# Optimization experiments

Measured on AMD Instinct MI355X. Metric: run time of the kernel, lower is better.

## Reference

```python
import jax, jax.numpy as jnp
import numpy as np
from jax.scipy.special import erf

# synthetic covalent radii table (original imports `covalent_radii`, e.g. from ase)
COV_RADII = jnp.asarray(0.3 + 0.02 * np.arange(100), dtype=jnp.float32)

B_MOL = 1024   # molecules per batch
N_ATOM = 128   # atoms per molecule (equal-sized ragged batch, atoms sorted by molecule)
N_ELEM = 10


def setup_inputs() -> dict:
    key = jax.random.key(0)
    ks = jax.random.split(key, 6)
    N = B_MOL * N_ATOM
    return {
        "eneg": jax.random.normal(ks[0], (N, 1), jnp.float32),
        "positions": jax.random.normal(ks[1], (N, 3), jnp.float32) * 3.0,
        "node_attrs": jax.random.uniform(ks[2], (N, N_ELEM), jnp.float32),
        "hardness": jax.random.uniform(ks[3], (N_ELEM,), jnp.float32),
        "total_charge": jax.random.normal(ks[4], (B_MOL,), jnp.float32),
        "batch": jnp.repeat(jnp.arange(B_MOL), N_ATOM),          # sorted molecule ids
        "atomic_numbers": jax.random.randint(ks[5], (N,), 1, 90),
    }


def reference(eneg, positions, node_attrs, hardness, total_charge, batch, atomic_numbers):
    # atoms are sorted by molecule with equal molecule sizes, so the ragged
    # python loop of the original collapses to a batched [B, n, ...] computation.
    B = total_charge.shape[0]
    N = positions.shape[0]
    n = N // B
    sqrt_pi = jnp.sqrt(jnp.asarray(np.pi, jnp.float32))
    sqrt_2 = jnp.sqrt(jnp.asarray(2.0, jnp.float32))

    pos = positions.reshape(B, n, 3)
    Z = atomic_numbers.reshape(B, n)
    atom_idx = jnp.argmax(node_attrs, axis=1).reshape(B, n)

    r = COV_RADII[Z]                                     # [B, n]
    diag_vals = hardness[atom_idx] + 1.0 / (sqrt_pi * r)  # [B, n]
    sigma = jnp.square(r)                                # [B, n]
    gamma = jnp.sqrt(sigma[:, :, None] + sigma[:, None, :])  # [B, n, n]

    diff = pos[:, :, None, :] - pos[:, None, :, :]       # [B, n, n, 3]
    sq = jnp.sum(diff * diff, axis=-1)                   # [B, n, n]
    eye = jnp.eye(n, dtype=bool)
    dist = jnp.sqrt(jnp.where(eye, 1.0, sq))             # safe diag (overwritten below)

    A = erf(dist / (sqrt_2 * gamma)) / dist              # [B, n, n]
    A = jnp.where(eye, diag_vals[:, :, None], A)         # scatter hardness diagonal

    # augment with charge-conservation row/column of ones (corner = 1)
    A = jnp.concatenate([A, jnp.ones((B, n, 1), A.dtype)], axis=2)
    A = jnp.concatenate([A, jnp.ones((B, 1, n + 1), A.dtype)], axis=1)

    b = jnp.concatenate([-eneg.reshape(B, n, 1),
                         total_charge.reshape(B, 1, 1)], axis=1)  # [B, n+1, 1]

    x = jnp.linalg.solve(A, b)                           # batched small solves
    return x[:, :n, 0].reshape(-1)                       # partial charges, [N]
```

## Files before the change

kernel.cpp:

```cpp
#include <hip/hip_runtime.h>
#include <math.h>

#define NMOL  1024
#define N     128
#define NELEM 10
#define BLOCK 256
#define PW    8
#define NPAN  16
#define PSTR  12
#define USTR  132

typedef __attribute__((ext_vector_type(4))) float f4;


__global__ __launch_bounds__(BLOCK, 2) void ceq_solve_kernel(
    const float* __restrict__ eneg,
    const float* __restrict__ positions,
    const float* __restrict__ node_attrs,
    const float* __restrict__ hardness,
    const float* __restrict__ total_charge,
    const int*   __restrict__ atomic_numbers,
    float* __restrict__ out)
{
    __shared__ __align__(16) float P[2][N * PSTR];
    __shared__ __align__(16) float Up[2][PW * USTR];
    __shared__ __align__(16) float Ublk[2][NPAN][PW][PW];
    __shared__ float rhsY[2][N], rhsZ[2][N];
    __shared__ float sxY[2][N], sxZ[2][N];
    __shared__ float px[2][N], py[2][N], pz[2][N], sg[2][N], dgv[2][N];
    __shared__ float lamS[2];

    const int tid  = threadIdx.x;
    const int lane = tid & 63;
    const int wid  = tid >> 6;
    const int g    = tid >> 7;
    const int wv   = wid & 1;
    const int gt   = tid & 127;
    const int r0   = 2 * lane;
    const int r1   = r0 + 1;
    const int col0 = 64 * wv;
    const int mol  = 2 * blockIdx.x + g;
    const int base = mol * N;

    {
        const int i = gt;
        const int Z = atomic_numbers[base + i];
        const float rad = 0.3f + 0.02f * (float)Z;
        sg[g][i] = rad * rad;
        const float* na = node_attrs + (size_t)(base + i) * NELEM;
        float best = na[0]; int bi = 0;
        #pragma unroll
        for (int e = 1; e < NELEM; ++e) {
            float v = na[e];
            if (v > best) { best = v; bi = e; }
        }
        dgv[g][i] = hardness[bi] + 0.5641895835477563f / rad;
        const float* p = positions + (size_t)(base + i) * 3;
        px[g][i] = p[0]; py[g][i] = p[1]; pz[g][i] = p[2];
        rhsY[g][i] = -eneg[base + i];
        rhsZ[g][i] = 1.0f;
    }
    __syncthreads();

    f4 Ar0[16], Ar1[16];
    {
        const float x0 = px[g][r0], y0 = py[g][r0], z0 = pz[g][r0];
        const float s0 = sg[g][r0], d0 = dgv[g][r0];
        #pragma unroll
        for (int c = 0; c < 16; ++c) {
            f4 v0;
            #pragma unroll
            for (int e = 0; e < 4; ++e) {
                const int j = col0 + 4 * c + e;
                float a0;
                if (j == r0) a0 = d0;
                else {
                    const float dx = x0 - px[g][j], dy = y0 - py[g][j], dz = z0 - pz[g][j];
                    const float d = sqrtf(dx * dx + dy * dy + dz * dz);
                    a0 = erff(d / (1.4142135623730951f * sqrtf(s0 + sg[g][j]))) / d;
                }
                ((float*)&v0)[e] = a0;
            }
            Ar0[c] = v0;
        }
        const float x1 = px[g][r1], y1 = py[g][r1], z1 = pz[g][r1];
        const float s1 = sg[g][r1], d1 = dgv[g][r1];
        #pragma unroll
        for (int c = 0; c < 16; ++c) {
            f4 v1;
            #pragma unroll
            for (int e = 0; e < 4; ++e) {
                const int j = col0 + 4 * c + e;
                float a1;
                if (j == r1) a1 = d1;
                else {
                    const float dx = x1 - px[g][j], dy = y1 - py[g][j], dz = z1 - pz[g][j];
                    const float d = sqrtf(dx * dx + dy * dy + dz * dz);
                    a1 = erff(d / (1.4142135623730951f * sqrtf(s1 + sg[g][j]))) / d;
                }
                ((float*)&v1)[e] = a1;
            }
            Ar1[c] = v1;
        }
    }

    for (int p = 0; p < NPAN; ++p) {
        const int k0   = PW * p;
        const int gclo = 2 * p + 2;
        const int q    = p & 7;

        if (wv == (p >> 3) && lane >= 4 * p) {
            f4 a00, a01, a10, a11;
            switch (q) {
                case 0:  a00 = Ar0[0];  a01 = Ar0[1];  a10 = Ar1[0];  a11 = Ar1[1];  break;
                case 1:  a00 = Ar0[2];  a01 = Ar0[3];  a10 = Ar1[2];  a11 = Ar1[3];  break;
                case 2:  a00 = Ar0[4];  a01 = Ar0[5];  a10 = Ar1[4];  a11 = Ar1[5];  break;
                case 3:  a00 = Ar0[6];  a01 = Ar0[7];  a10 = Ar1[6];  a11 = Ar1[7];  break;
                case 4:  a00 = Ar0[8];  a01 = Ar0[9];  a10 = Ar1[8];  a11 = Ar1[9];  break;
                case 5:  a00 = Ar0[10]; a01 = Ar0[11]; a10 = Ar1[10]; a11 = Ar1[11]; break;
                case 6:  a00 = Ar0[12]; a01 = Ar0[13]; a10 = Ar1[12]; a11 = Ar1[13]; break;
                default: a00 = Ar0[14]; a01 = Ar0[15]; a10 = Ar1[14]; a11 = Ar1[15]; break;
            }
            *(f4*)&P[g][r0 * PSTR + 0] = a00; *(f4*)&P[g][r0 * PSTR + 4] = a01;
            *(f4*)&P[g][r1 * PSTR + 0] = a10; *(f4*)&P[g][r1 * PSTR + 4] = a11;
        }
        if (lane >= 4 * p && lane < 4 * p + 4) {
            const int u0 = r0 - k0, u1 = u0 + 1;
            #pragma unroll
            for (int c = 0; c < 16; ++c) {
                const int gc = 16 * wv + c;
                if (gc >= gclo) {
                    *(f4*)&Up[g][u0 * USTR + 4 * gc] = Ar0[c];
                    *(f4*)&Up[g][u1 * USTR + 4 * gc] = Ar1[c];
                }
            }
        }
        if (gt < PW) {
            Up[g][gt * USTR + 128] = rhsY[g][k0 + gt];
            Up[g][gt * USTR + 129] = rhsZ[g][k0 + gt];
        }
        __syncthreads();

        if (wv == 0) {
            const int i0 = k0 + lane, i1 = i0 + 64;
            const bool v0 = i0 < N, v1 = i1 < N;
            float rg0[PW], rg1[PW];
            if (v0) {
                f4 a = *(const f4*)&P[g][i0 * PSTR], b = *(const f4*)&P[g][i0 * PSTR + 4];
                rg0[0]=a.x; rg0[1]=a.y; rg0[2]=a.z; rg0[3]=a.w;
                rg0[4]=b.x; rg0[5]=b.y; rg0[6]=b.z; rg0[7]=b.w;
            } else {
                #pragma unroll
                for (int j = 0; j < PW; ++j) rg0[j] = 0.0f;
            }
            if (v1) {
                f4 a = *(const f4*)&P[g][i1 * PSTR], b = *(const f4*)&P[g][i1 * PSTR + 4];
                rg1[0]=a.x; rg1[1]=a.y; rg1[2]=a.z; rg1[3]=a.w;
                rg1[4]=b.x; rg1[5]=b.y; rg1[6]=b.z; rg1[7]=b.w;
            } else {
                #pragma unroll
                for (int j = 0; j < PW; ++j) rg1[j] = 0.0f;
            }
            #pragma unroll
            for (int kk = 0; kk < PW; ++kk) {
                float pr[PW];
                #pragma unroll
                for (int j = kk; j < PW; ++j) pr[j] = __shfl(rg0[j], kk);
                const float dinv = 1.0f / pr[kk];
                if (v0 && i0 > k0 + kk) {
                    const float mult = rg0[kk] * dinv; rg0[kk] = mult;
                    #pragma unroll
                    for (int j = kk + 1; j < PW; ++j) rg0[j] -= mult * pr[j];
                }
                if (v1) {
                    const float mult = rg1[kk] * dinv; rg1[kk] = mult;
                    #pragma unroll
                    for (int j = kk + 1; j < PW; ++j) rg1[j] -= mult * pr[j];
                }
            }
            if (v0) {
                f4 a = { rg0[0], rg0[1], rg0[2], rg0[3] };
                f4 b = { rg0[4], rg0[5], rg0[6], rg0[7] };
                *(f4*)&P[g][i0 * PSTR] = a; *(f4*)&P[g][i0 * PSTR + 4] = b;
                if (lane < PW) {
                    *(f4*)&Ublk[g][p][lane][0] = a; *(f4*)&Ublk[g][p][lane][4] = b;
                }
            }
            if (v1) {
                f4 a = { rg1[0], rg1[1], rg1[2], rg1[3] };
                f4 b = { rg1[4], rg1[5], rg1[6], rg1[7] };
                *(f4*)&P[g][i1 * PSTR] = a; *(f4*)&P[g][i1 * PSTR + 4] = b;
            }
        }
        __syncthreads();

        const int ncols = 122 - k0;
        if (gt < ncols) {
            const int j = k0 + PW + gt;
            float u[PW];
            #pragma unroll
            for (int kk = 0; kk < PW; ++kk) u[kk] = Up[g][kk * USTR + j];
            #pragma unroll
            for (int kk = 1; kk < PW; ++kk) {
                float acc = u[kk];
                #pragma unroll
                for (int t = 0; t < kk; ++t) acc -= Ublk[g][p][kk][t] * u[t];
                u[kk] = acc;
            }
            #pragma unroll
            for (int kk = 0; kk < PW; ++kk) Up[g][kk * USTR + j] = u[kk];
        }
        __syncthreads();

        if (lane >= 4 * p && lane < 4 * p + 4) {
            const int u0 = r0 - k0, u1 = u0 + 1;
            #pragma unroll
            for (int c = 0; c < 16; ++c) {
                const int gc = 16 * wv + c;
                if (gc >= gclo) {
                    Ar0[c] = *(const f4*)&Up[g][u0 * USTR + 4 * gc];
                    Ar1[c] = *(const f4*)&Up[g][u1 * USTR + 4 * gc];
                }
            }
        }
        if (gt < PW) {
            rhsY[g][k0 + gt] = Up[g][gt * USTR + 128];
            rhsZ[g][k0 + gt] = Up[g][gt * USTR + 129];
        }
        const bool hasmat = (16 * wv + 15) >= gclo;
        if (lane >= 4 * p + 4) {
            float lA0[PW], lA1[PW];
            if (hasmat || wv == 0) {
                f4 a = *(const f4*)&P[g][r0 * PSTR], b = *(const f4*)&P[g][r0 * PSTR + 4];
                lA0[0]=a.x; lA0[1]=a.y; lA0[2]=a.z; lA0[3]=a.w;
                lA0[4]=b.x; lA0[5]=b.y; lA0[6]=b.z; lA0[7]=b.w;
                f4 c2 = *(const f4*)&P[g][r1 * PSTR], d2 = *(const f4*)&P[g][r1 * PSTR + 4];
                lA1[0]=c2.x; lA1[1]=c2.y; lA1[2]=c2.z; lA1[3]=c2.w;
                lA1[4]=d2.x; lA1[5]=d2.y; lA1[6]=d2.z; lA1[7]=d2.w;
            }
            if (hasmat) {
                #pragma unroll
                for (int c = 0; c < 16; ++c) {
                    const int gc = 16 * wv + c;
                    if (gc >= gclo) {
                        f4 acc0 = Ar0[c], acc1 = Ar1[c];
                        #pragma unroll
                        for (int u = 0; u < PW; ++u) {
                            const f4 uv = *(const f4*)&Up[g][u * USTR + 4 * gc];
                            acc0 -= uv * lA0[u];
                            acc1 -= uv * lA1[u];
                        }
                        Ar0[c] = acc0; Ar1[c] = acc1;
                    }
                }
            }
            if (wv == 0) {
                float yy0 = rhsY[g][r0], yy1 = rhsY[g][r1];
                float zz0 = rhsZ[g][r0], zz1 = rhsZ[g][r1];
                #pragma unroll
                for (int u = 0; u < PW; ++u) {
                    const float uy = Up[g][u * USTR + 128];
                    const float uz = Up[g][u * USTR + 129];
                    yy0 -= lA0[u] * uy; yy1 -= lA1[u] * uy;
                    zz0 -= lA0[u] * uz; zz1 -= lA1[u] * uz;
                }
                rhsY[g][r0] = yy0; rhsY[g][r1] = yy1;
                rhsZ[g][r0] = zz0; rhsZ[g][r1] = zz1;
            }
        }
        __syncthreads();
    }

    for (int pb = NPAN - 1; pb >= 0; --pb) {
        const int k0 = PW * pb;
        if (tid < 4) {
            const int gg = tid >> 1;
            float* rhs = (tid & 1) ? rhsZ[gg] : rhsY[gg];
            float* sx  = (tid & 1) ? sxZ[gg]  : sxY[gg];
            float x[PW];
            #pragma unroll
            for (int kk = PW - 1; kk >= 0; --kk) {
                float acc = rhs[k0 + kk];
                #pragma unroll
                for (int jj = kk + 1; jj < PW; ++jj) acc -= Ublk[gg][pb][kk][jj] * x[jj];
                x[kk] = acc / Ublk[gg][pb][kk][kk];
                sx[k0 + kk] = x[kk];
            }
        }
        __syncthreads();
        if (wv == (pb >> 3) && lane < 4 * pb) {
            f4 a00, a01, a10, a11;
            switch (pb & 7) {
                case 0:  a00 = Ar0[0];  a01 = Ar0[1];  a10 = Ar1[0];  a11 = Ar1[1];  break;
                case 1:  a00 = Ar0[2];  a01 = Ar0[3];  a10 = Ar1[2];  a11 = Ar1[3];  break;
                case 2:  a00 = Ar0[4];  a01 = Ar0[5];  a10 = Ar1[4];  a11 = Ar1[5];  break;
                case 3:  a00 = Ar0[6];  a01 = Ar0[7];  a10 = Ar1[6];  a11 = Ar1[7];  break;
                case 4:  a00 = Ar0[8];  a01 = Ar0[9];  a10 = Ar1[8];  a11 = Ar1[9];  break;
                case 5:  a00 = Ar0[10]; a01 = Ar0[11]; a10 = Ar1[10]; a11 = Ar1[11]; break;
                case 6:  a00 = Ar0[12]; a01 = Ar0[13]; a10 = Ar1[12]; a11 = Ar1[13]; break;
                default: a00 = Ar0[14]; a01 = Ar0[15]; a10 = Ar1[14]; a11 = Ar1[15]; break;
            }
            float yy0 = rhsY[g][r0], yy1 = rhsY[g][r1];
            float zz0 = rhsZ[g][r0], zz1 = rhsZ[g][r1];
            yy0 -= a00.x*sxY[g][k0]   + a00.y*sxY[g][k0+1] + a00.z*sxY[g][k0+2] + a00.w*sxY[g][k0+3]
                 + a01.x*sxY[g][k0+4] + a01.y*sxY[g][k0+5] + a01.z*sxY[g][k0+6] + a01.w*sxY[g][k0+7];
            yy1 -= a10.x*sxY[g][k0]   + a10.y*sxY[g][k0+1] + a10.z*sxY[g][k0+2] + a10.w*sxY[g][k0+3]
                 + a11.x*sxY[g][k0+4] + a11.y*sxY[g][k0+5] + a11.z*sxY[g][k0+6] + a11.w*sxY[g][k0+7];
            zz0 -= a00.x*sxZ[g][k0]   + a00.y*sxZ[g][k0+1] + a00.z*sxZ[g][k0+2] + a00.w*sxZ[g][k0+3]
                 + a01.x*sxZ[g][k0+4] + a01.y*sxZ[g][k0+5] + a01.z*sxZ[g][k0+6] + a01.w*sxZ[g][k0+7];
            zz1 -= a10.x*sxZ[g][k0]   + a10.y*sxZ[g][k0+1] + a10.z*sxZ[g][k0+2] + a10.w*sxZ[g][k0+3]
                 + a11.x*sxZ[g][k0+4] + a11.y*sxZ[g][k0+5] + a11.z*sxZ[g][k0+6] + a11.w*sxZ[g][k0+7];
            rhsY[g][r0] = yy0; rhsY[g][r1] = yy1;
            rhsZ[g][r0] = zz0; rhsZ[g][r1] = zz1;
        }
        __syncthreads();
    }

    if (wv == 0) {
        float vY = sxY[g][lane] + sxY[g][lane + 64];
        float vZ = sxZ[g][lane] + sxZ[g][lane + 64];
        #pragma unroll
        for (int off = 32; off; off >>= 1) {
            vY += __shfl_xor(vY, off);
            vZ += __shfl_xor(vZ, off);
        }
        if (lane == 0) lamS[g] = (vY - total_charge[mol]) / (vZ - 1.0f);
    }
    __syncthreads();
    out[base + gt] = sxY[g][gt] - lamS[g] * sxZ[g][gt];
}

extern "C" void kernel_launch(void* const* d_in, const int* in_sizes, int n_in,
                              void* d_out, int out_size, void* d_ws, size_t ws_size,
                              hipStream_t stream) {
    const float* eneg           = (const float*)d_in[0];
    const float* positions      = (const float*)d_in[1];
    const float* node_attrs     = (const float*)d_in[2];
    const float* hardness       = (const float*)d_in[3];
    const float* total_charge   = (const float*)d_in[4];
    const int*   atomic_numbers = (const int*)d_in[6];
    float* out = (float*)d_out;

    ceq_solve_kernel<<<NMOL / 2, BLOCK, 0, stream>>>(
        eneg, positions, node_attrs, hardness, total_charge, atomic_numbers, out);
}
```

Baseline: 226.3 us.

## Double-buffer panel and U-row staging to drop a barrier per panel step

Panel columns and next U rows are now written into a second shared buffer directly from the trailing update of the previous step. The separate staging phase and its __syncthreads at the top of each panel iteration go away. The right-hand sides are kept in registers instead of shared arrays, and the launch-bounds occupancy hint of 2 is removed. The cost is more shared memory for the doubled P/Up buffers and extra conditional stores inside the update loop.

```diff
diff --git a/kernel.cpp b/kernel.cpp
--- a/kernel.cpp
+++ b/kernel.cpp
@@ -13,7 +13,7 @@
 typedef __attribute__((ext_vector_type(4))) float f4;
 
 
-__global__ __launch_bounds__(BLOCK, 2) void ceq_solve_kernel(
+__global__ __launch_bounds__(BLOCK) void ceq_solve_kernel(
     const float* __restrict__ eneg,
     const float* __restrict__ positions,
     const float* __restrict__ node_attrs,
@@ -22,8 +22,8 @@
     const int*   __restrict__ atomic_numbers,
     float* __restrict__ out)
 {
-    __shared__ __align__(16) float P[2][N * PSTR];
-    __shared__ __align__(16) float Up[2][PW * USTR];
+    __shared__ __align__(16) float P[2][2][N * PSTR];
+    __shared__ __align__(16) float Up[2][2][PW * USTR];
     __shared__ __align__(16) float Ublk[2][NPAN][PW][PW];
     __shared__ float rhsY[2][N], rhsZ[2][N];
     __shared__ float sxY[2][N], sxZ[2][N];
@@ -57,9 +57,9 @@
         dgv[g][i] = hardness[bi] + 0.5641895835477563f / rad;
         const float* p = positions + (size_t)(base + i) * 3;
         px[g][i] = p[0]; py[g][i] = p[1]; pz[g][i] = p[2];
-        rhsY[g][i] = -eneg[base + i];
-        rhsZ[g][i] = 1.0f;
-    }
+    }
+    float rY0 = 0.f, rY1 = 0.f, rZ0 = 1.f, rZ1 = 1.f;
+    if (wv == 0) { rY0 = -eneg[base + r0]; rY1 = -eneg[base + r1]; }
     __syncthreads();
 
     f4 Ar0[16], Ar1[16];
@@ -104,59 +104,50 @@
         }
     }
 
+    if (wv == 0) {
+        *(f4*)&P[g][0][r0 * PSTR + 0] = Ar0[0]; *(f4*)&P[g][0][r0 * PSTR + 4] = Ar0[1];
+        *(f4*)&P[g][0][r1 * PSTR + 0] = Ar1[0]; *(f4*)&P[g][0][r1 * PSTR + 4] = Ar1[1];
+    }
+    if (lane < 4) {
+        #pragma unroll
+        for (int c = 0; c < 16; ++c) {
+            const int gc = 16 * wv + c;
+            if (gc >= 2) {
+                *(f4*)&Up[g][0][r0 * USTR + 4 * gc] = Ar0[c];
+                *(f4*)&Up[g][0][r1 * USTR + 4 * gc] = Ar1[c];
+            }
+        }
+        if (wv == 0) {
+            Up[g][0][r0 * USTR + 128] = rY0; Up[g][0][r1 * USTR + 128] = rY1;
+            Up[g][0][r0 * USTR + 129] = rZ0; Up[g][0][r1 * USTR + 129] = rZ1;
+        }
+    }
+    __syncthreads();
+
     for (int p = 0; p < NPAN; ++p) {
         const int k0   = PW * p;
         const int gclo = 2 * p + 2;
-        const int q    = p & 7;
-
-        if (wv == (p >> 3) && lane >= 4 * p) {
-            f4 a00, a01, a10, a11;
-            switch (q) {
-                case 0:  a00 = Ar0[0];  a01 = Ar0[1];  a10 = Ar1[0];  a11 = Ar1[1];  break;
-                case 1:  a00 = Ar0[2];  a01 = Ar0[3];  a10 = Ar1[2];  a11 = Ar1[3];  break;
-                case 2:  a00 = Ar0[4];  a01 = Ar0[5];  a10 = Ar1[4];  a11 = Ar1[5];  break;
-                case 3:  a00 = Ar0[6];  a01 = Ar0[7];  a10 = Ar1[6];  a11 = Ar1[7];  break;
-                case 4:  a00 = Ar0[8];  a01 = Ar0[9];  a10 = Ar1[8];  a11 = Ar1[9];  break;
-                case 5:  a00 = Ar0[10]; a01 = Ar0[11]; a10 = Ar1[10]; a11 = Ar1[11]; break;
-                case 6:  a00 = Ar0[12]; a01 = Ar0[13]; a10 = Ar1[12]; a11 = Ar1[13]; break;
-                default: a00 = Ar0[14]; a01 = Ar0[15]; a10 = Ar1[14]; a11 = Ar1[15]; break;
-            }
-            *(f4*)&P[g][r0 * PSTR + 0] = a00; *(f4*)&P[g][r0 * PSTR + 4] = a01;
-            *(f4*)&P[g][r1 * PSTR + 0] = a10; *(f4*)&P[g][r1 * PSTR + 4] = a11;
-        }
-        if (lane >= 4 * p && lane < 4 * p + 4) {
-            const int u0 = r0 - k0, u1 = u0 + 1;
-            #pragma unroll
-            for (int c = 0; c < 16; ++c) {
-                const int gc = 16 * wv + c;
-                if (gc >= gclo) {
-                    *(f4*)&Up[g][u0 * USTR + 4 * gc] = Ar0[c];
-                    *(f4*)&Up[g][u1 * USTR + 4 * gc] = Ar1[c];
-                }
-            }
-        }
-        if (gt < PW) {
-            Up[g][gt * USTR + 128] = rhsY[g][k0 + gt];
-            Up[g][gt * USTR + 129] = rhsZ[g][k0 + gt];
-        }
-        __syncthreads();
+        const int b    = p & 1;
+        const int bn   = b ^ 1;
+        const int pn   = p + 1;
+        const int k0n  = PW * pn;
 
         if (wv == 0) {
             const int i0 = k0 + lane, i1 = i0 + 64;
             const bool v0 = i0 < N, v1 = i1 < N;
             float rg0[PW], rg1[PW];
             if (v0) {
-                f4 a = *(const f4*)&P[g][i0 * PSTR], b = *(const f4*)&P[g][i0 * PSTR + 4];
+                f4 a = *(const f4*)&P[g][b][i0 * PSTR], b2 = *(const f4*)&P[g][b][i0 * PSTR + 4];
                 rg0[0]=a.x; rg0[1]=a.y; rg0[2]=a.z; rg0[3]=a.w;
-                rg0[4]=b.x; rg0[5]=b.y; rg0[6]=b.z; rg0[7]=b.w;
+                rg0[4]=b2.x; rg0[5]=b2.y; rg0[6]=b2.z; rg0[7]=b2.w;
             } else {
                 #pragma unroll
                 for (int j = 0; j < PW; ++j) rg0[j] = 0.0f;
             }
             if (v1) {
-                f4 a = *(const f4*)&P[g][i1 * PSTR], b = *(const f4*)&P[g][i1 * PSTR + 4];
+                f4 a = *(const f4*)&P[g][b][i1 * PSTR], b2 = *(const f4*)&P[g][b][i1 * PSTR + 4];
                 rg1[0]=a.x; rg1[1]=a.y; rg1[2]=a.z; rg1[3]=a.w;
-                rg1[4]=b.x; rg1[5]=b.y; rg1[6]=b.z; rg1[7]=b.w;
+                rg1[4]=b2.x; rg1[5]=b2.y; rg1[6]=b2.z; rg1[7]=b2.w;
             } else {
                 #pragma unroll
                 for (int j = 0; j < PW; ++j) rg1[j] = 0.0f;
@@ -180,16 +171,16 @@
             }
             if (v0) {
                 f4 a = { rg0[0], rg0[1], rg0[2], rg0[3] };
-                f4 b = { rg0[4], rg0[5], rg0[6], rg0[7] };
-                *(f4*)&P[g][i0 * PSTR] = a; *(f4*)&P[g][i0 * PSTR + 4] = b;
+                f4 b2 = { rg0[4], rg0[5], rg0[6], rg0[7] };
+                *(f4*)&P[g][b][i0 * PSTR] = a; *(f4*)&P[g][b][i0 * PSTR + 4] = b2;
                 if (lane < PW) {
-                    *(f4*)&Ublk[g][p][lane][0] = a; *(f4*)&Ublk[g][p][lane][4] = b;
+                    *(f4*)&Ublk[g][p][lane][0] = a; *(f4*)&Ublk[g][p][lane][4] = b2;
                 }
             }
             if (v1) {
                 f4 a = { rg1[0], rg1[1], rg1[2], rg1[3] };
-                f4 b = { rg1[4], rg1[5], rg1[6], rg1[7] };
-                *(f4*)&P[g][i1 * PSTR] = a; *(f4*)&P[g][i1 * PSTR + 4] = b;
+                f4 b2 = { rg1[4], rg1[5], rg1[6], rg1[7] };
+                *(f4*)&P[g][b][i1 * PSTR] = a; *(f4*)&P[g][b][i1 * PSTR + 4] = b2;
             }
         }
         __syncthreads();
@@ -199,7 +190,7 @@
             const int j = k0 + PW + gt;
             float u[PW];
             #pragma unroll
-            for (int kk = 0; kk < PW; ++kk) u[kk] = Up[g][kk * USTR + j];
+            for (int kk = 0; kk < PW; ++kk) u[kk] = Up[g][b][kk * USTR + j];
             #pragma unroll
             for (int kk = 1; kk < PW; ++kk) {
                 float acc = u[kk];
@@ -208,7 +199,7 @@
                 u[kk] = acc;
             }
             #pragma unroll
-            for (int kk = 0; kk < PW; ++kk) Up[g][kk * USTR + j] = u[kk];
+            for (int kk = 0; kk < PW; ++kk) Up[g][b][kk * USTR + j] = u[kk];
         }
         __syncthreads();
 
@@ -218,23 +209,24 @@
             for (int c = 0; c < 16; ++c) {
                 const int gc = 16 * wv + c;
                 if (gc >= gclo) {
-                    Ar0[c] = *(const f4*)&Up[g][u0 * USTR + 4 * gc];
-                    Ar1[c] = *(const f4*)&Up[g][u1 * USTR + 4 * gc];
+                    Ar0[c] = *(const f4*)&Up[g][b][u0 * USTR + 4 * gc];
+                    Ar1[c] = *(const f4*)&Up[g][b][u1 * USTR + 4 * gc];
                 }
             }
         }
         if (gt < PW) {
-            rhsY[g][k0 + gt] = Up[g][gt * USTR + 128];
-            rhsZ[g][k0 + gt] = Up[g][gt * USTR + 129];
+            rhsY[g][k0 + gt] = Up[g][b][gt * USTR + 128];
+            rhsZ[g][k0 + gt] = Up[g][b][gt * USTR + 129];
         }
         const bool hasmat = (16 * wv + 15) >= gclo;
+        const bool nown   = (lane >= 4 * pn && lane < 4 * pn + 4);
         if (lane >= 4 * p + 4) {
             float lA0[PW], lA1[PW];
             if (hasmat || wv == 0) {
-                f4 a = *(const f4*)&P[g][r0 * PSTR], b = *(const f4*)&P[g][r0 * PSTR + 4];
+                f4 a = *(const f4*)&P[g][b][r0 * PSTR], b2 = *(const f4*)&P[g][b][r0 * PSTR + 4];
                 lA0[0]=a.x; lA0[1]=a.y; lA0[2]=a.z; lA0[3]=a.w;
-                lA0[4]=b.x; lA0[5]=b.y; lA0[6]=b.z; lA0[7]=b.w;
-                f4 c2 = *(const f4*)&P[g][r1 * PSTR], d2 = *(const f4*)&P[g][r1 * PSTR + 4];
+                lA0[4]=b2.x; lA0[5]=b2.y; lA0[6]=b2.z; lA0[7]=b2.w;
+                f4 c2 = *(const f4*)&P[g][b][r1 * PSTR], d2 = *(const f4*)&P[g][b][r1 * PSTR + 4];
                 lA1[0]=c2.x; lA1[1]=c2.y; lA1[2]=c2.z; lA1[3]=c2.w;
                 lA1[4]=d2.x; lA1[5]=d2.y; lA1[6]=d2.z; lA1[7]=d2.w;
             }
@@ -246,26 +238,40 @@
                         f4 acc0 = Ar0[c], acc1 = Ar1[c];
                         #pragma unroll
                         for (int u = 0; u < PW; ++u) {
-                            const f4 uv = *(const f4*)&Up[g][u * USTR + 4 * gc];
+                            const f4 uv = *(const f4*)&Up[g][b][u * USTR + 4 * gc];
                             acc0 -= uv * lA0[u];
                             acc1 -= uv * lA1[u];
                         }
                         Ar0[c] = acc0; Ar1[c] = acc1;
+                        if (p < NPAN - 1) {
+                            if (gc == 2 * pn) {
+                                *(f4*)&P[g][bn][r0 * PSTR + 0] = acc0;
+                                *(f4*)&P[g][bn][r1 * PSTR + 0] = acc1;
+                            } else if (gc == 2 * pn + 1) {
+                                *(f4*)&P[g][bn][r0 * PSTR + 4] = acc0;
+                                *(f4*)&P[g][bn][r1 * PSTR + 4] = acc1;
+                            } else if (nown) {
+                                *(f4*)&Up[g][bn][(r0 - k0n) * USTR + 4 * gc] = acc0;
+                                *(f4*)&Up[g][bn][(r1 - k0n) * USTR + 4 * gc] = acc1;
+                            }
+                        }
                     }
                 }
             }
             if (wv == 0) {
-                float yy0 = rhsY[g][r0], yy1 = rhsY[g][r1];
-                float zz0 = rhsZ[g][r0], zz1 = rhsZ[g][r1];
                 #pragma unroll
                 for (int u = 0; u < PW; ++u) {
-                    const float uy = Up[g][u * USTR + 128];
-                    const float uz = Up[g][u * USTR + 129];
-                    yy0 -= lA0[u] * uy; yy1 -= lA1[u] * uy;
-                    zz0 -= lA0[u] * uz; zz1 -= lA1[u] * uz;
-                }
-                rhsY[g][r0] = yy0; rhsY[g][r1] = yy1;
-                rhsZ[g][r0] = zz0; rhsZ[g][r1] = zz1;
+                    const float uy = Up[g][b][u * USTR + 128];
+                    const float uz = Up[g][b][u * USTR + 129];
+                    rY0 -= lA0[u] * uy; rY1 -= lA1[u] * uy;
+                    rZ0 -= lA0[u] * uz; rZ1 -= lA1[u] * uz;
+                }
+                if (p < NPAN - 1 && nown) {
+                    Up[g][bn][(r0 - k0n) * USTR + 128] = rY0;
+                    Up[g][bn][(r1 - k0n) * USTR + 128] = rY1;
+                    Up[g][bn][(r0 - k0n) * USTR + 129] = rZ0;
+                    Up[g][bn][(r1 - k0n) * USTR + 129] = rZ1;
+                }
             }
         }
         __syncthreads();
```

Measured after the change: 335.6 us. 48.3% more time.

## Spill first four matrix column-chunks to LDS and factor panel from U-row copy

Applied to the files above, without the earlier changes.

Moves the first 4 of 16 per-thread f4 column chunks of the in-register matrix into shared memory, so fewer registers are held and occupancy or spill behaviour may improve. It also drops the P panel buffer. The 8x8 diagonal block is now factored by 8 lanes reading the already-published U rows, and the L multipliers are rebuilt from the transposed U row times stored reciprocal pivots. The cost is extra LDS traffic for the spilled chunks and per-row multiplier loads, plus a slightly altered elimination structure.

```diff
diff --git a/kernel.cpp b/kernel.cpp
--- a/kernel.cpp
+++ b/kernel.cpp
@@ -7,7 +7,6 @@
 #define BLOCK 256
 #define PW    8
 #define NPAN  16
-#define PSTR  12
 #define USTR  132
 
 typedef __attribute__((ext_vector_type(4))) float f4;
@@ -22,9 +21,11 @@
     const int*   __restrict__ atomic_numbers,
     float* __restrict__ out)
 {
-    __shared__ __align__(16) float P[2][N * PSTR];
+    __shared__ __align__(16) f4    Aex0[4][BLOCK];
+    __shared__ __align__(16) f4    Aex1[4][BLOCK];
     __shared__ __align__(16) float Up[2][PW * USTR];
     __shared__ __align__(16) float Ublk[2][NPAN][PW][PW];
+    __shared__ float dinvS[2][PW];
     __shared__ float rhsY[2][N], rhsZ[2][N];
     __shared__ float sxY[2][N], sxZ[2][N];
     __shared__ float px[2][N], py[2][N], pz[2][N], sg[2][N], dgv[2][N];
@@ -62,7 +63,7 @@
     }
     __syncthreads();
 
-    f4 Ar0[16], Ar1[16];
+    f4 Ar0[12], Ar1[12];
     {
         const float x0 = px[g][r0], y0 = py[g][r0], z0 = pz[g][r0];
         const float s0 = sg[g][r0], d0 = dgv[g][r0];
@@ -81,7 +82,7 @@
                 }
                 ((float*)&v0)[e] = a0;
             }
-            Ar0[c] = v0;
+            if (c < 4) Aex0[c][tid] = v0; else Ar0[c - 4] = v0;
         }
         const float x1 = px[g][r1], y1 = py[g][r1], z1 = pz[g][r1];
         const float s1 = sg[g][r1], d1 = dgv[g][r1];
@@ -100,38 +101,31 @@
                 }
                 ((float*)&v1)[e] = a1;
             }
-            Ar1[c] = v1;
-        }
-    }
+            if (c < 4) Aex1[c][tid] = v1; else Ar1[c - 4] = v1;
+        }
+    }
+    __syncthreads();
 
     for (int p = 0; p < NPAN; ++p) {
         const int k0   = PW * p;
         const int gclo = 2 * p + 2;
-        const int q    = p & 7;
-
-        if (wv == (p >> 3) && lane >= 4 * p) {
-            f4 a00, a01, a10, a11;
-            switch (q) {
-                case 0:  a00 = Ar0[0];  a01 = Ar0[1];  a10 = Ar1[0];  a11 = Ar1[1];  break;
-                case 1:  a00 = Ar0[2];  a01 = Ar0[3];  a10 = Ar1[2];  a11 = Ar1[3];  break;
-                case 2:  a00 = Ar0[4];  a01 = Ar0[5];  a10 = Ar1[4];  a11 = Ar1[5];  break;
-                case 3:  a00 = Ar0[6];  a01 = Ar0[7];  a10 = Ar1[6];  a11 = Ar1[7];  break;
-                case 4:  a00 = Ar0[8];  a01 = Ar0[9];  a10 = Ar1[8];  a11 = Ar1[9];  break;
-                case 5:  a00 = Ar0[10]; a01 = Ar0[11]; a10 = Ar1[10]; a11 = Ar1[11]; break;
-                case 6:  a00 = Ar0[12]; a01 = Ar0[13]; a10 = Ar1[12]; a11 = Ar1[13]; break;
-                default: a00 = Ar0[14]; a01 = Ar0[15]; a10 = Ar1[14]; a11 = Ar1[15]; break;
-            }
-            *(f4*)&P[g][r0 * PSTR + 0] = a00; *(f4*)&P[g][r0 * PSTR + 4] = a01;
-            *(f4*)&P[g][r1 * PSTR + 0] = a10; *(f4*)&P[g][r1 * PSTR + 4] = a11;
-        }
+
         if (lane >= 4 * p && lane < 4 * p + 4) {
             const int u0 = r0 - k0, u1 = u0 + 1;
             #pragma unroll
-            for (int c = 0; c < 16; ++c) {
+            for (int c = 0; c < 4; ++c) {
                 const int gc = 16 * wv + c;
-                if (gc >= gclo) {
-                    *(f4*)&Up[g][u0 * USTR + 4 * gc] = Ar0[c];
-                    *(f4*)&Up[g][u1 * USTR + 4 * gc] = Ar1[c];
+                if (gc >= 2 * p) {
+                    *(f4*)&Up[g][u0 * USTR + 4 * gc] = Aex0[c][tid];
+                    *(f4*)&Up[g][u1 * USTR + 4 * gc] = Aex1[c][tid];
+                }
+            }
+            #pragma unroll
+            for (int c = 4; c < 16; ++c) {
+                const int gc = 16 * wv + c;
+                if (gc >= 2 * p) {
+                    *(f4*)&Up[g][u0 * USTR + 4 * gc] = Ar0[c - 4];
+                    *(f4*)&Up[g][u1 * USTR + 4 * gc] = Ar1[c - 4];
                 }
             }
         }
@@ -141,56 +135,25 @@
         }
         __syncthreads();
 
-        if (wv == 0) {
-            const int i0 = k0 + lane, i1 = i0 + 64;
-            const bool v0 = i0 < N, v1 = i1 < N;
-            float rg0[PW], rg1[PW];
-            if (v0) {
-                f4 a = *(const f4*)&P[g][i0 * PSTR], b = *(const f4*)&P[g][i0 * PSTR + 4];
-                rg0[0]=a.x; rg0[1]=a.y; rg0[2]=a.z; rg0[3]=a.w;
-                rg0[4]=b.x; rg0[5]=b.y; rg0[6]=b.z; rg0[7]=b.w;
-            } else {
-                #pragma unroll
-                for (int j = 0; j < PW; ++j) rg0[j] = 0.0f;
-            }
-            if (v1) {
-                f4 a = *(const f4*)&P[g][i1 * PSTR], b = *(const f4*)&P[g][i1 * PSTR + 4];
-                rg1[0]=a.x; rg1[1]=a.y; rg1[2]=a.z; rg1[3]=a.w;
-                rg1[4]=b.x; rg1[5]=b.y; rg1[6]=b.z; rg1[7]=b.w;
-            } else {
-                #pragma unroll
-                for (int j = 0; j < PW; ++j) rg1[j] = 0.0f;
-            }
+        if (wv == 0 && lane < PW) {
+            float v[PW];
+            #pragma unroll
+            for (int t = 0; t < PW; ++t) v[t] = Up[g][lane * USTR + k0 + t];
             #pragma unroll
             for (int kk = 0; kk < PW; ++kk) {
                 float pr[PW];
                 #pragma unroll
-                for (int j = kk; j < PW; ++j) pr[j] = __shfl(rg0[j], kk);
-                const float dinv = 1.0f / pr[kk];
-                if (v0 && i0 > k0 + kk) {
-                    const float mult = rg0[kk] * dinv; rg0[kk] = mult;
+                for (int j = kk; j < PW; ++j) pr[j] = __shfl(v[j], kk);
+                if (lane > kk) {
+                    const float mult = v[kk] / pr[kk];
+                    v[kk] = mult;
                     #pragma unroll
-                    for (int j = kk + 1; j < PW; ++j) rg0[j] -= mult * pr[j];
-                }
-                if (v1) {
-                    const float mult = rg1[kk] * dinv; rg1[kk] = mult;
-                    #pragma unroll
-                    for (int j = kk + 1; j < PW; ++j) rg1[j] -= mult * pr[j];
-                }
-            }
-            if (v0) {
-                f4 a = { rg0[0], rg0[1], rg0[2], rg0[3] };
-                f4 b = { rg0[4], rg0[5], rg0[6], rg0[7] };
-                *(f4*)&P[g][i0 * PSTR] = a; *(f4*)&P[g][i0 * PSTR + 4] = b;
-                if (lane < PW) {
-                    *(f4*)&Ublk[g][p][lane][0] = a; *(f4*)&Ublk[g][p][lane][4] = b;
-                }
-            }
-            if (v1) {
-                f4 a = { rg1[0], rg1[1], rg1[2], rg1[3] };
-                f4 b = { rg1[4], rg1[5], rg1[6], rg1[7] };
-                *(f4*)&P[g][i1 * PSTR] = a; *(f4*)&P[g][i1 * PSTR + 4] = b;
-            }
+                    for (int j = kk + 1; j < PW; ++j) v[j] -= mult * pr[j];
+                }
+            }
+            #pragma unroll
+            for (int t = 0; t < PW; ++t) Ublk[g][p][lane][t] = v[t];
+            dinvS[g][lane] = 1.0f / v[lane];
         }
         __syncthreads();
 
@@ -215,11 +178,19 @@
         if (lane >= 4 * p && lane < 4 * p + 4) {
             const int u0 = r0 - k0, u1 = u0 + 1;
             #pragma unroll
-            for (int c = 0; c < 16; ++c) {
+            for (int c = 0; c < 4; ++c) {
                 const int gc = 16 * wv + c;
                 if (gc >= gclo) {
-                    Ar0[c] = *(const f4*)&Up[g][u0 * USTR + 4 * gc];
-                    Ar1[c] = *(const f4*)&Up[g][u1 * USTR + 4 * gc];
+                    Aex0[c][tid] = *(const f4*)&Up[g][u0 * USTR + 4 * gc];
+                    Aex1[c][tid] = *(const f4*)&Up[g][u1 * USTR + 4 * gc];
+                }
+            }
+            #pragma unroll
+            for (int c = 4; c < 16; ++c) {
+                const int gc = 16 * wv + c;
+                if (gc >= gclo) {
+                    Ar0[c - 4] = *(const f4*)&Up[g][u0 * USTR + 4 * gc];
+                    Ar1[c - 4] = *(const f4*)&Up[g][u1 * USTR + 4 * gc];
                 }
             }
         }
@@ -231,26 +202,40 @@
         if (lane >= 4 * p + 4) {
             float lA0[PW], lA1[PW];
             if (hasmat || wv == 0) {
-                f4 a = *(const f4*)&P[g][r0 * PSTR], b = *(const f4*)&P[g][r0 * PSTR + 4];
-                lA0[0]=a.x; lA0[1]=a.y; lA0[2]=a.z; lA0[3]=a.w;
-                lA0[4]=b.x; lA0[5]=b.y; lA0[6]=b.z; lA0[7]=b.w;
-                f4 c2 = *(const f4*)&P[g][r1 * PSTR], d2 = *(const f4*)&P[g][r1 * PSTR + 4];
-                lA1[0]=c2.x; lA1[1]=c2.y; lA1[2]=c2.z; lA1[3]=c2.w;
-                lA1[4]=d2.x; lA1[5]=d2.y; lA1[6]=d2.z; lA1[7]=d2.w;
+                #pragma unroll
+                for (int u = 0; u < PW; ++u) {
+                    const float du = dinvS[g][u];
+                    lA0[u] = Up[g][u * USTR + r0] * du;
+                    lA1[u] = Up[g][u * USTR + r1] * du;
+                }
             }
             if (hasmat) {
                 #pragma unroll
-                for (int c = 0; c < 16; ++c) {
+                for (int c = 0; c < 4; ++c) {
                     const int gc = 16 * wv + c;
                     if (gc >= gclo) {
-                        f4 acc0 = Ar0[c], acc1 = Ar1[c];
+                        f4 acc0 = Aex0[c][tid], acc1 = Aex1[c][tid];
                         #pragma unroll
                         for (int u = 0; u < PW; ++u) {
                             const f4 uv = *(const f4*)&Up[g][u * USTR + 4 * gc];
                             acc0 -= uv * lA0[u];
                             acc1 -= uv * lA1[u];
                         }
-                        Ar0[c] = acc0; Ar1[c] = acc1;
+                        Aex0[c][tid] = acc0; Aex1[c][tid] = acc1;
+                    }
+                }
+                #pragma unroll
+                for (int c = 4; c < 16; ++c) {
+                    const int gc = 16 * wv + c;
+                    if (gc >= gclo) {
+                        f4 acc0 = Ar0[c - 4], acc1 = Ar1[c - 4];
+                        #pragma unroll
+                        for (int u = 0; u < PW; ++u) {
+                            const f4 uv = *(const f4*)&Up[g][u * USTR + 4 * gc];
+                            acc0 -= uv * lA0[u];
+                            acc1 -= uv * lA1[u];
+                        }
+                        Ar0[c - 4] = acc0; Ar1[c - 4] = acc1;
                     }
                 }
             }
@@ -291,14 +276,16 @@
         if (wv == (pb >> 3) && lane < 4 * pb) {
             f4 a00, a01, a10, a11;
             switch (pb & 7) {
-                case 0:  a00 = Ar0[0];  a01 = Ar0[1];  a10 = Ar1[0];  a11 = Ar1[1];  break;
-                case 1:  a00 = Ar0[2];  a01 = Ar0[3];  a10 = Ar1[2];  a11 = Ar1[3];  break;
-                case 2:  a00 = Ar0[4];  a01 = Ar0[5];  a10 = Ar1[4];  a11 = Ar1[5];  break;
-                case 3:  a00 = Ar0[6];  a01 = Ar0[7];  a10 = Ar1[6];  a11 = Ar1[7];  break;
-                case 4:  a00 = Ar0[8];  a01 = Ar0[9];  a10 = Ar1[8];  a11 = Ar1[9];  break;
-                case 5:  a00 = Ar0[10]; a01 = Ar0[11]; a10 = Ar1[10]; a11 = Ar1[11]; break;
-                case 6:  a00 = Ar0[12]; a01 = Ar0[13]; a10 = Ar1[12]; a11 = Ar1[13]; break;
-                default: a00 = Ar0[14]; a01 = Ar0[15]; a10 = Ar1[14]; a11 = Ar1[15]; break;
+                case 0:  a00 = Aex0[0][tid]; a01 = Aex0[1][tid];
+                         a10 = Aex1[0][tid]; a11 = Aex1[1][tid]; break;
+                case 1:  a00 = Aex0[2][tid]; a01 = Aex0[3][tid];
+                         a10 = Aex1[2][tid]; a11 = Aex1[3][tid]; break;
+                case 2:  a00 = Ar0[0];  a01 = Ar0[1];  a10 = Ar1[0];  a11 = Ar1[1];  break;
+                case 3:  a00 = Ar0[2];  a01 = Ar0[3];  a10 = Ar1[2];  a11 = Ar1[3];  break;
+                case 4:  a00 = Ar0[4];  a01 = Ar0[5];  a10 = Ar1[4];  a11 = Ar1[5];  break;
+                case 5:  a00 = Ar0[6];  a01 = Ar0[7];  a10 = Ar1[6];  a11 = Ar1[7];  break;
+                case 6:  a00 = Ar0[8];  a01 = Ar0[9];  a10 = Ar1[8];  a11 = Ar1[9];  break;
+                default: a00 = Ar0[10]; a01 = Ar0[11]; a10 = Ar1[10]; a11 = Ar1[11]; break;
             }
             float yy0 = rhsY[g][r0], yy1 = rhsY[g][r1];
             float zz0 = rhsZ[g][r0], zz1 = rhsZ[g][r1];
```

Result: slower. 304.9 us (+34.8%).
